# Performance work log

Hardware: AMD Instinct MI355X
Metric: run time of the kernel (lower is better)

The kernel has to match this reference:

```python
import jax, jax.numpy as jnp
import numpy as np

D_PRIME = 512
D = 2048
CLASSES = 4


def setup_inputs() -> dict:
    key = jax.random.key(0)
    k1, k2, k3, k4 = jax.random.split(key, 4)
    N = 32768
    V_prime = jax.random.normal(k1, (N, D), dtype=jnp.float32)
    U_t = jax.random.normal(k2, (D_PRIME, D), dtype=jnp.float32)
    W_mta = jax.random.normal(k3, (1, D_PRIME), dtype=jnp.float32)
    W = jax.random.normal(k4, (CLASSES, D), dtype=jnp.float32)
    return {"V_prime": V_prime, "U_t": U_t, "W_mta": W_mta, "W": W}


def reference(V_prime, U_t, W_mta, W):
    # [D_prime, N] = tanh(U_t @ V'^T)
    tanh_scores = jnp.tanh(U_t @ V_prime.T)
    # attention over instances: [1, N]
    a = jax.nn.softmax(W_mta @ tanh_scores, axis=1)
    # weighted sum pooling: [D]
    t = jnp.sum(a.T * V_prime, axis=0)
    # final linear: [1, classes]
    l = (W @ t).reshape(1, CLASSES)
    return l
```

## Files before the change

### kernel.cpp

```cpp
#include <hip/hip_runtime.h>

#define N_INST 32768
#define DIM    2048
#define DP     512
#define NCLS   4

typedef _Float16 half8_t __attribute__((ext_vector_type(8)));
typedef float    float4_t __attribute__((ext_vector_type(4)));

#define OFF_VHI   0ull
#define OFF_UHI   (OFF_VHI  + (size_t)N_INST*DIM*2)
#define OFF_S     (OFF_UHI  + (size_t)DP*DIM*2)
#define OFF_STAT  (OFF_S    + (size_t)N_INST*4)
#define OFF_PSTAT (OFF_STAT + 256ull)
#define OFF_PART  (OFF_PSTAT+ 256ull)

#define GLOAD_LDS16(g, l) __builtin_amdgcn_global_load_lds( \
    (__attribute__((address_space(1))) void*)(g),           \
    (__attribute__((address_space(3))) void*)(l), 16, 0, 0)

__device__ __forceinline__ float tanh_fast(float x) {
  float e = __expf(2.0f * x);
  return 1.0f - 2.0f / (e + 1.0f);
}

__global__ __launch_bounds__(256) void k_cvt(const float4* __restrict__ in,
                                             half8_t* __restrict__ out) {
  int i = blockIdx.x * 256 + threadIdx.x;
  float4 a = in[2 * i], b = in[2 * i + 1];
  half8_t h;
  h[0] = (_Float16)a.x; h[1] = (_Float16)a.y;
  h[2] = (_Float16)a.z; h[3] = (_Float16)a.w;
  h[4] = (_Float16)b.x; h[5] = (_Float16)b.y;
  h[6] = (_Float16)b.z; h[7] = (_Float16)b.w;
  out[i] = h;
}

__global__ __launch_bounds__(256, 4) void k_score_gemm(
    const _Float16* __restrict__ Uhi, const _Float16* __restrict__ Vhi,
    const float* __restrict__ Wmta, float* __restrict__ s) {
  __shared__ _Float16 lA[2][128 * 32];
  __shared__ _Float16 lB[2][128 * 32];

  const int tid = threadIdx.x;
  const int lane = tid & 63;
  const int wv = tid >> 6;
  const int waveM = wv >> 1;
  const int waveN = wv & 1;
  const int quad = lane >> 4;
  const int col = lane & 15;

  const int b = blockIdx.x;
  const int grp = b >> 5;
  const int win = b & 31;
  const int mb = win >> 3;
  const int nb = grp * 8 + (win & 7);

  const int aRow0 = mb * 128;
  const int bRow0 = nb * 128;

  float4_t acc[4][4];
  const float4_t z4 = {0.f, 0.f, 0.f, 0.f};
  for (int i = 0; i < 4; i++)
    for (int j = 0; j < 4; j++) acc[i][j] = z4;

  const int stR = tid >> 2;
  const int stC = (tid & 3) << 3;

  const _Float16* gA0 = Uhi + (size_t)(aRow0 + stR) * DIM + stC;
  const _Float16* gA1 = Uhi + (size_t)(aRow0 + 64 + stR) * DIM + stC;
  const _Float16* gB0 = Vhi + (size_t)(bRow0 + stR) * DIM + stC;
  const _Float16* gB1 = Vhi + (size_t)(bRow0 + 64 + stR) * DIM + stC;
  const int lbase0 = (wv << 6) << 3;
  const int lbase1 = (256 + (wv << 6)) << 3;

  GLOAD_LDS16(gA0, &lA[0][lbase0]);
  GLOAD_LDS16(gA1, &lA[0][lbase1]);
  GLOAD_LDS16(gB0, &lB[0][lbase0]);
  GLOAD_LDS16(gB1, &lB[0][lbase1]);

  for (int ki = 0; ki < 64; ++ki) {
    const int cur = ki & 1, nxt = cur ^ 1;
    __syncthreads();

    if (ki + 1 < 64) {
      const int kn = (ki + 1) << 5;
      GLOAD_LDS16(gA0 + kn, &lA[nxt][lbase0]);
      GLOAD_LDS16(gA1 + kn, &lA[nxt][lbase1]);
      GLOAD_LDS16(gB0 + kn, &lB[nxt][lbase0]);
      GLOAD_LDS16(gB1 + kn, &lB[nxt][lbase1]);
    }

    half8_t af[4], bf[4];
    for (int mi = 0; mi < 4; mi++) {
      const int row = waveM * 64 + mi * 16 + col;
      af[mi] = *(const half8_t*)&lA[cur][row * 32 + quad * 8];
    }
    for (int ni = 0; ni < 4; ni++) {
      const int row = waveN * 64 + ni * 16 + col;
      bf[ni] = *(const half8_t*)&lB[cur][row * 32 + quad * 8];
    }
    for (int mi = 0; mi < 4; mi++)
      for (int ni = 0; ni < 4; ni++)
        acc[mi][ni] = __builtin_amdgcn_mfma_f32_16x16x32_f16(af[mi], bf[ni], acc[mi][ni], 0, 0, 0);
  }

  for (int ni = 0; ni < 4; ni++) {
    float v = 0.0f;
    for (int mi = 0; mi < 4; mi++) {
      const int jb = aRow0 + waveM * 64 + mi * 16 + quad * 4;
      union { float4_t v4; float f[4]; } u;
      u.v4 = acc[mi][ni];
      for (int r = 0; r < 4; r++)
        v += Wmta[jb + r] * tanh_fast(u.f[r]);
    }
    v += __shfl_xor(v, 16);
    v += __shfl_xor(v, 32);
    if (quad == 0) {
      const int n = bRow0 + waveN * 64 + ni * 16 + col;
      atomicAdd(&s[n], v);
    }
  }
}

__global__ __launch_bounds__(256) void k_stats1(const float* __restrict__ s,
                                                float* __restrict__ pstat) {
  const int tid = threadIdx.x;
  const int lane = tid & 63;
  const int wvi = tid >> 6;
  __shared__ float smM[4], smP[4];
  const float4* s4 = (const float4*)s;

  float4 v = s4[blockIdx.x * 256 + tid];
  float m = fmaxf(fmaxf(v.x, v.y), fmaxf(v.z, v.w));
  float p = __expf(v.x - m) + __expf(v.y - m) + __expf(v.z - m) + __expf(v.w - m);
  for (int o = 32; o > 0; o >>= 1) {
    float om = __shfl_xor(m, o);
    float op = __shfl_xor(p, o);
    float nm = fmaxf(m, om);
    p = p * __expf(m - nm) + op * __expf(om - nm);
    m = nm;
  }
  if (lane == 0) { smM[wvi] = m; smP[wvi] = p; }
  __syncthreads();
  if (tid == 0) {
    float gm = fmaxf(fmaxf(smM[0], smM[1]), fmaxf(smM[2], smM[3]));
    float sum = 0.f;
    for (int w = 0; w < 4; w++) sum += smP[w] * __expf(smM[w] - gm);
    pstat[blockIdx.x * 2]     = gm;
    pstat[blockIdx.x * 2 + 1] = sum;
  }
}

__global__ __launch_bounds__(64) void k_stats2(const float* __restrict__ pstat,
                                               float* __restrict__ stats) {
  const int tid = threadIdx.x;
  float m = -3.4e38f, p = 0.0f;
  if (tid < 32) { m = pstat[tid * 2]; p = pstat[tid * 2 + 1]; }
  for (int o = 32; o > 0; o >>= 1) {
    float om = __shfl_xor(m, o);
    float op = __shfl_xor(p, o);
    float nm = fmaxf(m, om);
    p = p * __expf(m - nm) + op * __expf(om - nm);
    m = nm;
  }
  if (tid == 0) { stats[0] = m; stats[1] = 1.0f / p; }
}

__global__ __launch_bounds__(256) void k_pool(const float* __restrict__ V,
                                              const float* __restrict__ s,
                                              const float* __restrict__ stats,
                                              float* __restrict__ part) {
  const int tid = threadIdx.x;
  const float mx = stats[0], inv = stats[1];
  const int n0 = blockIdx.x * 128;
  float acc[8] = {0.f, 0.f, 0.f, 0.f, 0.f, 0.f, 0.f, 0.f};
  for (int r = 0; r < 128; ++r) {
    const int n = n0 + r;
    const float w = __expf(s[n] - mx) * inv;
    if (w > 1e-12f) {
      const float4* vp = (const float4*)&V[(size_t)n * DIM + tid * 8];
      float4 va = vp[0], vb = vp[1];
      acc[0] += w * va.x; acc[1] += w * va.y; acc[2] += w * va.z; acc[3] += w * va.w;
      acc[4] += w * vb.x; acc[5] += w * vb.y; acc[6] += w * vb.z; acc[7] += w * vb.w;
    }
  }
  float* dst = &part[(size_t)blockIdx.x * DIM + tid * 8];
  *(float4*)(dst + 0) = make_float4(acc[0], acc[1], acc[2], acc[3]);
  *(float4*)(dst + 4) = make_float4(acc[4], acc[5], acc[6], acc[7]);
}

__global__ __launch_bounds__(256) void k_reduce_final(const float* __restrict__ part,
                                                      const float* __restrict__ W,
                                                      float* __restrict__ out) {
  const int d = blockIdx.x * 256 + threadIdx.x;
  float t = 0.f;
  for (int bb = 0; bb < 256; ++bb) t += part[(size_t)bb * DIM + d];

  float pc[NCLS];
#pragma unroll
  for (int c = 0; c < NCLS; ++c) pc[c] = W[(size_t)c * DIM + d] * t;

  __shared__ float sred[4][NCLS];
  const int lane = threadIdx.x & 63;
  const int wvi = threadIdx.x >> 6;
#pragma unroll
  for (int c = 0; c < NCLS; ++c)
    for (int o = 32; o > 0; o >>= 1) pc[c] += __shfl_xor(pc[c], o);
  if (lane == 0)
    for (int c = 0; c < NCLS; ++c) sred[wvi][c] = pc[c];
  __syncthreads();
  if (threadIdx.x < NCLS) {
    float v = sred[0][threadIdx.x] + sred[1][threadIdx.x] +
              sred[2][threadIdx.x] + sred[3][threadIdx.x];
    atomicAdd(&out[threadIdx.x], v);
  }
}

extern "C" void kernel_launch(void* const* d_in, const int* in_sizes, int n_in,
                              void* d_out, int out_size, void* d_ws, size_t ws_size,
                              hipStream_t stream) {
  const float* Vp   = (const float*)d_in[0];
  const float* Ut   = (const float*)d_in[1];
  const float* Wmta = (const float*)d_in[2];
  const float* W    = (const float*)d_in[3];
  float* out = (float*)d_out;

  char* ws = (char*)d_ws;
  _Float16* Vhi  = (_Float16*)(ws + OFF_VHI);
  _Float16* Uhi  = (_Float16*)(ws + OFF_UHI);
  float*    sBuf = (float*)(ws + OFF_S);
  float*    stat = (float*)(ws + OFF_STAT);
  float*    pstat= (float*)(ws + OFF_PSTAT);
  float*    partB= (float*)(ws + OFF_PART);

  hipMemsetAsync(sBuf, 0, (size_t)N_INST * 4, stream);
  hipMemsetAsync(out, 0, (size_t)NCLS * 4, stream);

  k_cvt<<<(N_INST * DIM / 8) / 256, 256, 0, stream>>>((const float4*)Vp, (half8_t*)Vhi);
  k_cvt<<<(DP * DIM / 8) / 256, 256, 0, stream>>>((const float4*)Ut, (half8_t*)Uhi);
  k_score_gemm<<<(DP / 128) * (N_INST / 128), 256, 0, stream>>>(Uhi, Vhi, Wmta, sBuf);
  k_stats1<<<32, 256, 0, stream>>>(sBuf, pstat);
  k_stats2<<<1, 64, 0, stream>>>(pstat, stat);
  k_pool<<<N_INST / 128, 256, 0, stream>>>(Vp, sBuf, stat, partB);
  k_reduce_final<<<DIM / 256, 256, 0, stream>>>(partB, W, out);
}
```

Measured before the change: 494.0 us.

## Fuse V fp32-to-fp16 conversion into score GEMM B-tile loading

Removes the separate conversion kernel for V' and instead has the score GEMM load fp32 V rows into registers two k-steps ahead, convert to fp16, and store into LDS. This drops a full read of V plus a 128MB fp16 write and its re-read. In exchange, each of the four M-blocks rereads fp32 V (twice the bytes of fp16), and the B path moves from direct global-to-LDS loads to register staging, which adds register pressure and VALU conversion work.

```diff
diff --git a/kernel.cpp b/kernel.cpp
--- a/kernel.cpp
+++ b/kernel.cpp
@@ -8,8 +8,7 @@
 typedef _Float16 half8_t __attribute__((ext_vector_type(8)));
 typedef float    float4_t __attribute__((ext_vector_type(4)));
 
-#define OFF_VHI   0ull
-#define OFF_UHI   (OFF_VHI  + (size_t)N_INST*DIM*2)
+#define OFF_UHI   0ull
 #define OFF_S     (OFF_UHI  + (size_t)DP*DIM*2)
 #define OFF_STAT  (OFF_S    + (size_t)N_INST*4)
 #define OFF_PSTAT (OFF_STAT + 256ull)
@@ -37,7 +36,7 @@
 }
 
 __global__ __launch_bounds__(256, 4) void k_score_gemm(
-    const _Float16* __restrict__ Uhi, const _Float16* __restrict__ Vhi,
+    const _Float16* __restrict__ Uhi, const float* __restrict__ V,
     const float* __restrict__ Wmta, float* __restrict__ s) {
   __shared__ _Float16 lA[2][128 * 32];
   __shared__ _Float16 lB[2][128 * 32];
@@ -65,30 +64,63 @@
     for (int j = 0; j < 4; j++) acc[i][j] = z4;
 
   const int stR = tid >> 2;
-  const int stC = (tid & 3) << 3;
-
-  const _Float16* gA0 = Uhi + (size_t)(aRow0 + stR) * DIM + stC;
-  const _Float16* gA1 = Uhi + (size_t)(aRow0 + 64 + stR) * DIM + stC;
-  const _Float16* gB0 = Vhi + (size_t)(bRow0 + stR) * DIM + stC;
-  const _Float16* gB1 = Vhi + (size_t)(bRow0 + 64 + stR) * DIM + stC;
+  const int stQ = (tid & 3) << 3;
+
+  const _Float16* gA0 = Uhi + (size_t)(aRow0 + stR) * DIM + stQ;
+  const _Float16* gA1 = Uhi + (size_t)(aRow0 + 64 + stR) * DIM + stQ;
+  const float*    gB0 = V   + (size_t)(bRow0 + stR) * DIM + stQ;
+  const float*    gB1 = V   + (size_t)(bRow0 + 64 + stR) * DIM + stQ;
   const int lbase0 = (wv << 6) << 3;
   const int lbase1 = (256 + (wv << 6)) << 3;
 
+  float4 rb[2][4];
+
+  rb[0][0] = *(const float4*)(gB0);      rb[0][1] = *(const float4*)(gB0 + 4);
+  rb[0][2] = *(const float4*)(gB1);      rb[0][3] = *(const float4*)(gB1 + 4);
+  rb[1][0] = *(const float4*)(gB0 + 32); rb[1][1] = *(const float4*)(gB0 + 36);
+  rb[1][2] = *(const float4*)(gB1 + 32); rb[1][3] = *(const float4*)(gB1 + 36);
   GLOAD_LDS16(gA0, &lA[0][lbase0]);
   GLOAD_LDS16(gA1, &lA[0][lbase1]);
-  GLOAD_LDS16(gB0, &lB[0][lbase0]);
-  GLOAD_LDS16(gB1, &lB[0][lbase1]);
+  {
+    half8_t h0, h1;
+    h0[0] = (_Float16)rb[0][0].x; h0[1] = (_Float16)rb[0][0].y;
+    h0[2] = (_Float16)rb[0][0].z; h0[3] = (_Float16)rb[0][0].w;
+    h0[4] = (_Float16)rb[0][1].x; h0[5] = (_Float16)rb[0][1].y;
+    h0[6] = (_Float16)rb[0][1].z; h0[7] = (_Float16)rb[0][1].w;
+    h1[0] = (_Float16)rb[0][2].x; h1[1] = (_Float16)rb[0][2].y;
+    h1[2] = (_Float16)rb[0][2].z; h1[3] = (_Float16)rb[0][2].w;
+    h1[4] = (_Float16)rb[0][3].x; h1[5] = (_Float16)rb[0][3].y;
+    h1[6] = (_Float16)rb[0][3].z; h1[7] = (_Float16)rb[0][3].w;
+    *(half8_t*)&lB[0][stR * 32 + stQ] = h0;
+    *(half8_t*)&lB[0][(stR + 64) * 32 + stQ] = h1;
+  }
 
   for (int ki = 0; ki < 64; ++ki) {
     const int cur = ki & 1, nxt = cur ^ 1;
     __syncthreads();
 
     if (ki + 1 < 64) {
+      half8_t h0, h1;
+      h0[0] = (_Float16)rb[nxt][0].x; h0[1] = (_Float16)rb[nxt][0].y;
+      h0[2] = (_Float16)rb[nxt][0].z; h0[3] = (_Float16)rb[nxt][0].w;
+      h0[4] = (_Float16)rb[nxt][1].x; h0[5] = (_Float16)rb[nxt][1].y;
+      h0[6] = (_Float16)rb[nxt][1].z; h0[7] = (_Float16)rb[nxt][1].w;
+      h1[0] = (_Float16)rb[nxt][2].x; h1[1] = (_Float16)rb[nxt][2].y;
+      h1[2] = (_Float16)rb[nxt][2].z; h1[3] = (_Float16)rb[nxt][2].w;
+      h1[4] = (_Float16)rb[nxt][3].x; h1[5] = (_Float16)rb[nxt][3].y;
+      h1[6] = (_Float16)rb[nxt][3].z; h1[7] = (_Float16)rb[nxt][3].w;
+      *(half8_t*)&lB[nxt][stR * 32 + stQ] = h0;
+      *(half8_t*)&lB[nxt][(stR + 64) * 32 + stQ] = h1;
       const int kn = (ki + 1) << 5;
       GLOAD_LDS16(gA0 + kn, &lA[nxt][lbase0]);
       GLOAD_LDS16(gA1 + kn, &lA[nxt][lbase1]);
-      GLOAD_LDS16(gB0 + kn, &lB[nxt][lbase0]);
-      GLOAD_LDS16(gB1 + kn, &lB[nxt][lbase1]);
+    }
+    if (ki + 2 < 64) {
+      const int kp = (ki + 2) << 5;
+      rb[cur][0] = *(const float4*)(gB0 + kp);
+      rb[cur][1] = *(const float4*)(gB0 + kp + 4);
+      rb[cur][2] = *(const float4*)(gB1 + kp);
+      rb[cur][3] = *(const float4*)(gB1 + kp + 4);
     }
 
     half8_t af[4], bf[4];
@@ -227,7 +259,6 @@
   float* out = (float*)d_out;
 
   char* ws = (char*)d_ws;
-  _Float16* Vhi  = (_Float16*)(ws + OFF_VHI);
   _Float16* Uhi  = (_Float16*)(ws + OFF_UHI);
   float*    sBuf = (float*)(ws + OFF_S);
   float*    stat = (float*)(ws + OFF_STAT);
@@ -237,9 +268,8 @@
   hipMemsetAsync(sBuf, 0, (size_t)N_INST * 4, stream);
   hipMemsetAsync(out, 0, (size_t)NCLS * 4, stream);
 
-  k_cvt<<<(N_INST * DIM / 8) / 256, 256, 0, stream>>>((const float4*)Vp, (half8_t*)Vhi);
   k_cvt<<<(DP * DIM / 8) / 256, 256, 0, stream>>>((const float4*)Ut, (half8_t*)Uhi);
-  k_score_gemm<<<(DP / 128) * (N_INST / 128), 256, 0, stream>>>(Uhi, Vhi, Wmta, sBuf);
+  k_score_gemm<<<(DP / 128) * (N_INST / 128), 256, 0, stream>>>(Uhi, Vp, Wmta, sBuf);
   k_stats1<<<32, 256, 0, stream>>>(sBuf, pstat);
   k_stats2<<<1, 64, 0, stream>>>(pstat, stat);
   k_pool<<<N_INST / 128, 256, 0, stream>>>(Vp, sBuf, stat, partB);
```

Result: slower. 781.2 us (+58.1%).
